# Optimization experiments

Measured on AMD Instinct MI355X. Metric: run time of the kernel, lower is better.

## Reference

```python
import jax, jax.numpy as jnp
from jax import lax
import numpy as np

B, C, H, W = 16, 192, 128, 128
NF = 192


def hard_sigmoid(x):
    # Keras 1.x hard_sigmoid: clip(0.2*x + 0.5, 0, 1)
    return jnp.clip(0.2 * x + 0.5, 0.0, 1.0)


def setup_inputs() -> dict:
    key = jax.random.key(0)
    k1, k2, k3 = jax.random.split(key, 3)
    x = jax.random.normal(k1, (B, C, H, W), dtype=jnp.float32)
    W_iof = jax.random.normal(k2, (4 * NF, C, 1, 1), dtype=jnp.float32) * 0.05
    U_iof = jax.random.normal(k3, (4 * NF, NF, 3, 1), dtype=jnp.float32) * 0.05
    b_iof = jnp.zeros((4 * NF,), dtype=jnp.float32)
    init_h = jnp.zeros((NF, W), dtype=jnp.float32)
    init_c = jnp.zeros((NF, W), dtype=jnp.float32)
    return {"x": x, "W_iof": W_iof, "U_iof": U_iof, "b_iof": b_iof,
            "init_h": init_h, "init_c": init_c}


def reference(x, W_iof, U_iof, b_iof, init_h, init_c):
    b, c, h_dim, w_dim = x.shape
    nf = init_h.shape[0]
    in3 = c // 3
    out3 = nf // 3
    # pyramid channel mask on the 1x1 input-to-state weights
    mask = jnp.ones((4 * nf, c), dtype=x.dtype)
    mask = mask.at[:out3, in3:].set(0.0)
    mask = mask.at[out3:2 * out3, 2 * in3:].set(0.0)
    Wm = W_iof[:, :, 0, 0] * mask  # (4nf, c)
    U = U_iof[:, :, :, 0]          # (4nf, nf, 3)

    # direction 'Down': scan over rows (H). Precompute input-to-state for all rows.
    X = jnp.transpose(x, (0, 2, 1, 3))  # (B, H, C, W)
    i2s = jnp.einsum('bhcw,oc->bhow', X, Wm) + b_iof[None, None, :, None]  # (B,H,4nf,W)

    h0 = jnp.broadcast_to(init_h[None], (b, nf, w_dim))
    c0 = jnp.broadcast_to(init_c[None], (b, nf, w_dim))

    def step(carry, its):
        h_tm1, c_tm1 = carry
        # 3-wide cross-correlation along W, 'half' padding (lax conv is correlation)
        s2s = lax.conv_general_dilated(h_tm1, U, (1,), [(1, 1)],
                                       dimension_numbers=('NCH', 'OIH', 'NCH'))
        gates = its + s2s  # (B, 4nf, W)
        ofi = hard_sigmoid(gates[:, :3 * nf])
        o = ofi[:, :nf]
        f = ofi[:, nf:2 * nf]
        i = ofi[:, 2 * nf:3 * nf]
        g = jnp.tanh(gates[:, 3 * nf:])
        c_new = f * c_tm1 + i * g
        h_new = o * jnp.tanh(c_new)
        return (h_new, c_new), h_new

    _, hs = lax.scan(step, (h0, c0), jnp.transpose(i2s, (1, 0, 2, 3)))  # (H,B,nf,W)
    # return_sequences=True then permute (0,2,1,3): (B, H, nf, W) -> (B, nf, H, W)
    return jnp.transpose(hs, (1, 2, 0, 3))
```

## Files before the change

### kernel.cpp

```cpp
#include <hip/hip_runtime.h>
#include <math.h>

#define BB 16
#define CC 192
#define NF 192
#define HH 128
#define WW 128
#define G4 768
#define KTOT 768
#define LDA 776
#define NJB 12
#define GRIDSZ (NJB * BB)
#define SMEM_BYTES ((64 * LDA + 128 * 24) * 2)

typedef __bf16 bf16x8 __attribute__((ext_vector_type(8)));
typedef float  f32x4  __attribute__((ext_vector_type(4)));

__device__ unsigned g_cnt[BB * 64];

__device__ __forceinline__ float hsig(float v) {
    float y = fmaf(0.2f, v, 0.5f);
    return fminf(fmaxf(y, 0.f), 1.f);
}

__device__ __forceinline__ float tanh_fast(float x) {
    float y = fminf(fmaxf(x, -8.f), 8.f) * 2.885390082f;
    float e = __builtin_amdgcn_exp2f(y);
    float r = __builtin_amdgcn_rcpf(e + 1.f);
    return fmaf(-2.f, r, 1.f);
}

__device__ __forceinline__ unsigned short f2bf(float f) {
    unsigned int u = __float_as_uint(f);
    u += 0x7fffu + ((u >> 16) & 1u);
    return (unsigned short)(u >> 16);
}

__global__ void prep_weights(const float* __restrict__ Wf,
                             const float* __restrict__ Uf,
                             unsigned short* __restrict__ Wc) {
    int idx = blockIdx.x * blockDim.x + threadIdx.x;
    if (idx < BB)
        g_cnt[idx * 64] = 0u;
    if (idx >= G4 * KTOT) return;
    int row = idx / KTOT;
    int k   = idx - row * KTOT;
    float v;
    if (k < CC) {
        int lim = row < 64 ? 64 : (row < 128 ? 128 : 192);
        v = (k < lim) ? Wf[row * CC + k] : 0.f;
    } else {
        int kp = k - CC;
        int d  = kp / CC;
        int c  = kp - d * CC;
        v = Uf[((size_t)row * CC + c) * 3 + d];
    }
    Wc[idx] = f2bf(v);
}

__global__ void prep_bx(const float* __restrict__ x, unsigned short* __restrict__ Bsrc) {
    int idx = blockIdx.x * blockDim.x + threadIdx.x;
    if (idx >= HH * BB * WW) return;
    int w = idx & (WW - 1);
    int r = idx >> 7;
    int b = r & (BB - 1);
    int t = r >> 4;
    const float* xp = x + ((size_t)b * CC * HH + t) * WW + w;
    unsigned short* dp = Bsrc + (size_t)idx * KTOT;
#pragma unroll
    for (int cc = 0; cc < CC / 8; ++cc) {
        unsigned short v[8];
#pragma unroll
        for (int i = 0; i < 8; ++i)
            v[i] = f2bf(xp[(size_t)(cc * 8 + i) * (HH * WW)]);
        *(uint4*)(dp + cc * 8) = *(uint4*)v;
    }
}

__global__ void prep_bh_oob(unsigned short* __restrict__ Bsrc) {
    int idx = blockIdx.x * blockDim.x + threadIdx.x;
    if (idx >= HH * BB * 384) return;
    int u = idx % 384;
    int r = idx / 384;
    int b = r & (BB - 1);
    int t = r >> 4;
    size_t base = ((size_t)(t * BB + b) * WW) * KTOT;
    size_t off = (u < 192) ? (size_t)0 * KTOT + 192 + u
                           : (size_t)127 * KTOT + 384 + u;
    Bsrc[base + off] = 0;
}

__global__ void prep_bh0(const float* __restrict__ init_h, unsigned short* __restrict__ Bsrc) {
    int idx = blockIdx.x * blockDim.x + threadIdx.x;
    if (idx >= BB * WW * 576) return;
    int kp = idx % 576;
    int r  = idx / 576;
    int w  = r & (WW - 1);
    int b  = r >> 7;
    int d  = kp / CC;
    int c  = kp - d * CC;
    int wt = w + d - 1;
    float v = (wt >= 0 && wt < WW) ? init_h[c * WW + wt] : 0.f;
    Bsrc[((size_t)b * WW + w) * KTOT + CC + kp] = f2bf(v);
}

__global__ __launch_bounds__(512, 1) void lstm_persist(
    const unsigned short* __restrict__ Wc,
    unsigned short* __restrict__ Bsrc,
    const float* __restrict__ bias,
    const float* __restrict__ init_c,
    float* __restrict__ out)
{
    extern __shared__ unsigned short smem[];
    unsigned short (*Alds)[LDA] = (unsigned short(*)[LDA])smem;
    unsigned short (*hT)[24]    = (unsigned short(*)[24])(smem + 64 * LDA);

    const int tid  = threadIdx.x;
    const int nw   = tid >> 6;
    const int lane = tid & 63;
    const int m    = lane & 15;
    const int q    = lane >> 4;
    const int jb   = blockIdx.x % NJB;
    const int b    = blockIdx.x / NJB;
    const int j0   = jb * 16;
    const int w    = nw * 16 + m;
    unsigned* const cntp = &g_cnt[b * 64];

    for (int u = tid; u < 64 * 96; u += 512) {
        int r  = u / 96;
        int ko = (u - r * 96) * 8;
        int grow = (r >> 4) * NF + j0 + (r & 15);
        *(uint4*)&Alds[r][ko] = *(const uint4*)(Wc + (size_t)grow * KTOT + ko);
    }
    float breg[4][4];
#pragma unroll
    for (int g = 0; g < 4; ++g)
#pragma unroll
        for (int r = 0; r < 4; ++r)
            breg[g][r] = bias[g * NF + j0 + q * 4 + r];
    float creg[4];
#pragma unroll
    for (int r = 0; r < 4; ++r)
        creg[r] = init_c[(j0 + q * 4 + r) * WW + w];
    __syncthreads();

    for (int t = 0; t < HH; ++t) {
        f32x4 acc[4];
#pragma unroll
        for (int g = 0; g < 4; ++g)
            acc[g] = (f32x4){breg[g][0], breg[g][1], breg[g][2], breg[g][3]};

        const unsigned short* Bn =
            Bsrc + ((size_t)(t * BB + b) * WW + w) * KTOT;

        bf16x8 bx[6];
#pragma unroll
        for (int kc = 0; kc < 6; ++kc)
            bx[kc] = *(const bf16x8*)(Bn + kc * 32 + q * 8);
#pragma unroll
        for (int kc = 0; kc < 6; ++kc) {
            const int k = kc * 32 + q * 8;
            bf16x8 a0 = *(const bf16x8*)&Alds[ 0 + m][k];
            bf16x8 a1 = *(const bf16x8*)&Alds[16 + m][k];
            bf16x8 a2 = *(const bf16x8*)&Alds[32 + m][k];
            bf16x8 a3 = *(const bf16x8*)&Alds[48 + m][k];
            acc[0] = __builtin_amdgcn_mfma_f32_16x16x32_bf16(a0, bx[kc], acc[0], 0, 0, 0);
            acc[1] = __builtin_amdgcn_mfma_f32_16x16x32_bf16(a1, bx[kc], acc[1], 0, 0, 0);
            acc[2] = __builtin_amdgcn_mfma_f32_16x16x32_bf16(a2, bx[kc], acc[2], 0, 0, 0);
            acc[3] = __builtin_amdgcn_mfma_f32_16x16x32_bf16(a3, bx[kc], acc[3], 0, 0, 0);
        }

        if (t > 0) {
            const unsigned need = (unsigned)(NJB * t);
            while (__hip_atomic_load(cntp, __ATOMIC_RELAXED,
                                     __HIP_MEMORY_SCOPE_AGENT) < need)
                __builtin_amdgcn_s_sleep(1);
            __builtin_amdgcn_fence(__ATOMIC_ACQUIRE, "workgroup");
        }

        bf16x8 bh[18];
#pragma unroll
        for (int kc = 0; kc < 18; ++kc)
            bh[kc] = *(const bf16x8*)(Bn + 192 + kc * 32 + q * 8);
#pragma unroll
        for (int kc = 0; kc < 18; ++kc) {
            const int k = 192 + kc * 32 + q * 8;
            bf16x8 a0 = *(const bf16x8*)&Alds[ 0 + m][k];
            bf16x8 a1 = *(const bf16x8*)&Alds[16 + m][k];
            bf16x8 a2 = *(const bf16x8*)&Alds[32 + m][k];
            bf16x8 a3 = *(const bf16x8*)&Alds[48 + m][k];
            acc[0] = __builtin_amdgcn_mfma_f32_16x16x32_bf16(a0, bh[kc], acc[0], 0, 0, 0);
            acc[1] = __builtin_amdgcn_mfma_f32_16x16x32_bf16(a1, bh[kc], acc[1], 0, 0, 0);
            acc[2] = __builtin_amdgcn_mfma_f32_16x16x32_bf16(a2, bh[kc], acc[2], 0, 0, 0);
            acc[3] = __builtin_amdgcn_mfma_f32_16x16x32_bf16(a3, bh[kc], acc[3], 0, 0, 0);
        }

#pragma unroll
        for (int r = 0; r < 4; ++r) {
            const int j = j0 + q * 4 + r;
            float og = hsig(acc[0][r]);
            float fg = hsig(acc[1][r]);
            float ig = hsig(acc[2][r]);
            float gg = tanh_fast(acc[3][r]);
            float cn = fmaf(fg, creg[r], ig * gg);
            creg[r] = cn;
            float hn = og * tanh_fast(cn);
            out[(((size_t)b * NF + j) * HH + t) * WW + w] = hn;
            hT[w][q * 4 + r] = f2bf(hn);
        }
        __syncthreads();

        if (t < HH - 1) {
            unsigned short* Bns = Bsrc + ((size_t)((t + 1) * BB + b) * WW) * KTOT;
            if (tid < 384) {
                int d  = tid >> 7;
                int w2 = tid & 127;
                int ws = w2 + d - 1;
                if (ws >= 0 && ws < WW) {
                    const unsigned long long* s8 =
                        (const unsigned long long*)&hT[ws][0];
                    unsigned long long* d8 = (unsigned long long*)
                        (Bns + (size_t)w2 * KTOT + CC + d * CC + j0);
#pragma unroll
                    for (int e = 0; e < 4; ++e)
                        __hip_atomic_store(d8 + e, s8[e], __ATOMIC_RELAXED,
                                           __HIP_MEMORY_SCOPE_AGENT);
                }
            }
            __syncthreads();
            if (tid == 0)
                __hip_atomic_fetch_add(cntp, 1u, __ATOMIC_RELAXED,
                                       __HIP_MEMORY_SCOPE_AGENT);
        }
    }
}

extern "C" void kernel_launch(void* const* d_in, const int* in_sizes, int n_in,
                              void* d_out, int out_size, void* d_ws, size_t ws_size,
                              hipStream_t stream) {
    const float* x      = (const float*)d_in[0];
    const float* W_iof  = (const float*)d_in[1];
    const float* U_iof  = (const float*)d_in[2];
    const float* b_iof  = (const float*)d_in[3];
    const float* init_h = (const float*)d_in[4];
    const float* init_c = (const float*)d_in[5];
    float* out = (float*)d_out;

    unsigned short* Wc   = (unsigned short*)d_ws;
    unsigned short* Bsrc = Wc + (size_t)G4 * KTOT;

    prep_weights<<<(G4 * KTOT + 255) / 256, 256, 0, stream>>>(W_iof, U_iof, Wc);
    prep_bx<<<(HH * BB * WW + 255) / 256, 256, 0, stream>>>(x, Bsrc);
    prep_bh_oob<<<(HH * BB * 384 + 255) / 256, 256, 0, stream>>>(Bsrc);
    prep_bh0<<<(BB * WW * 576 + 255) / 256, 256, 0, stream>>>(init_h, Bsrc);

    const unsigned short* Wcp = Wc;
    unsigned short* Bsp = Bsrc;
    const float* bp = b_iof;
    const float* icp = init_c;
    float* op = out;
    void* args[] = {&Wcp, &Bsp, &bp, &icp, &op};
    hipLaunchCooperativeKernel((const void*)lstm_persist, dim3(GRIDSZ), dim3(512),
                               args, SMEM_BYTES, stream);
}
```

Measured before the change: 1.765 ms.

## Scatter h directly from registers, prefetch next-step input, defer output store

Each thread now packs its four bf16 h values and writes them straight to the three shifted positions in the next step's B buffer. This removes the LDS staging array and one __syncthreads per step. The input-projection operand for the next timestep is prefetched into registers during the current step, and the fp32 output store is moved after the counter increment so it is off the critical path. The added s_waitcnt before the barrier keeps visibility ordering, at the cost of more scattered 8-byte global stores and more registers in use.

```diff
diff --git a/kernel.cpp b/kernel.cpp
--- a/kernel.cpp
+++ b/kernel.cpp
@@ -11,7 +11,7 @@
 #define LDA 776
 #define NJB 12
 #define GRIDSZ (NJB * BB)
-#define SMEM_BYTES ((64 * LDA + 128 * 24) * 2)
+#define SMEM_BYTES (64 * LDA * 2)
 
 typedef __bf16 bf16x8 __attribute__((ext_vector_type(8)));
 typedef float  f32x4  __attribute__((ext_vector_type(4)));
@@ -113,7 +113,6 @@
 {
     extern __shared__ unsigned short smem[];
     unsigned short (*Alds)[LDA] = (unsigned short(*)[LDA])smem;
-    unsigned short (*hT)[24]    = (unsigned short(*)[24])(smem + 64 * LDA);
 
     const int tid  = threadIdx.x;
     const int nw   = tid >> 6;
@@ -144,6 +143,14 @@
         creg[r] = init_c[(j0 + q * 4 + r) * WW + w];
     __syncthreads();
 
+    bf16x8 bxc[6], bxn[6];
+    {
+        const unsigned short* B0 = Bsrc + ((size_t)b * WW + w) * KTOT;
+#pragma unroll
+        for (int kc = 0; kc < 6; ++kc)
+            bxc[kc] = *(const bf16x8*)(B0 + kc * 32 + q * 8);
+    }
+
     for (int t = 0; t < HH; ++t) {
         f32x4 acc[4];
 #pragma unroll
@@ -153,10 +160,6 @@
         const unsigned short* Bn =
             Bsrc + ((size_t)(t * BB + b) * WW + w) * KTOT;
 
-        bf16x8 bx[6];
-#pragma unroll
-        for (int kc = 0; kc < 6; ++kc)
-            bx[kc] = *(const bf16x8*)(Bn + kc * 32 + q * 8);
 #pragma unroll
         for (int kc = 0; kc < 6; ++kc) {
             const int k = kc * 32 + q * 8;
@@ -164,10 +167,10 @@
             bf16x8 a1 = *(const bf16x8*)&Alds[16 + m][k];
             bf16x8 a2 = *(const bf16x8*)&Alds[32 + m][k];
             bf16x8 a3 = *(const bf16x8*)&Alds[48 + m][k];
-            acc[0] = __builtin_amdgcn_mfma_f32_16x16x32_bf16(a0, bx[kc], acc[0], 0, 0, 0);
-            acc[1] = __builtin_amdgcn_mfma_f32_16x16x32_bf16(a1, bx[kc], acc[1], 0, 0, 0);
-            acc[2] = __builtin_amdgcn_mfma_f32_16x16x32_bf16(a2, bx[kc], acc[2], 0, 0, 0);
-            acc[3] = __builtin_amdgcn_mfma_f32_16x16x32_bf16(a3, bx[kc], acc[3], 0, 0, 0);
+            acc[0] = __builtin_amdgcn_mfma_f32_16x16x32_bf16(a0, bxc[kc], acc[0], 0, 0, 0);
+            acc[1] = __builtin_amdgcn_mfma_f32_16x16x32_bf16(a1, bxc[kc], acc[1], 0, 0, 0);
+            acc[2] = __builtin_amdgcn_mfma_f32_16x16x32_bf16(a2, bxc[kc], acc[2], 0, 0, 0);
+            acc[3] = __builtin_amdgcn_mfma_f32_16x16x32_bf16(a3, bxc[kc], acc[3], 0, 0, 0);
         }
 
         if (t > 0) {
@@ -182,6 +185,14 @@
 #pragma unroll
         for (int kc = 0; kc < 18; ++kc)
             bh[kc] = *(const bf16x8*)(Bn + 192 + kc * 32 + q * 8);
+
+        if (t < HH - 1) {
+            const unsigned short* Bx = Bn + (size_t)BB * WW * KTOT;
+#pragma unroll
+            for (int kc = 0; kc < 6; ++kc)
+                bxn[kc] = *(const bf16x8*)(Bx + kc * 32 + q * 8);
+        }
+
 #pragma unroll
         for (int kc = 0; kc < 18; ++kc) {
             const int k = 192 + kc * 32 + q * 8;
@@ -195,43 +206,52 @@
             acc[3] = __builtin_amdgcn_mfma_f32_16x16x32_bf16(a3, bh[kc], acc[3], 0, 0, 0);
         }
 
+        float hn[4];
 #pragma unroll
         for (int r = 0; r < 4; ++r) {
-            const int j = j0 + q * 4 + r;
             float og = hsig(acc[0][r]);
             float fg = hsig(acc[1][r]);
             float ig = hsig(acc[2][r]);
             float gg = tanh_fast(acc[3][r]);
             float cn = fmaf(fg, creg[r], ig * gg);
             creg[r] = cn;
-            float hn = og * tanh_fast(cn);
-            out[(((size_t)b * NF + j) * HH + t) * WW + w] = hn;
-            hT[w][q * 4 + r] = f2bf(hn);
-        }
-        __syncthreads();
+            hn[r] = og * tanh_fast(cn);
+        }
 
         if (t < HH - 1) {
-            unsigned short* Bns = Bsrc + ((size_t)((t + 1) * BB + b) * WW) * KTOT;
-            if (tid < 384) {
-                int d  = tid >> 7;
-                int w2 = tid & 127;
-                int ws = w2 + d - 1;
-                if (ws >= 0 && ws < WW) {
-                    const unsigned long long* s8 =
-                        (const unsigned long long*)&hT[ws][0];
-                    unsigned long long* d8 = (unsigned long long*)
-                        (Bns + (size_t)w2 * KTOT + CC + d * CC + j0);
-#pragma unroll
-                    for (int e = 0; e < 4; ++e)
-                        __hip_atomic_store(d8 + e, s8[e], __ATOMIC_RELAXED,
-                                           __HIP_MEMORY_SCOPE_AGENT);
-                }
-            }
+            unsigned long long pk =
+                  (unsigned long long)f2bf(hn[0])
+                | ((unsigned long long)f2bf(hn[1]) << 16)
+                | ((unsigned long long)f2bf(hn[2]) << 32)
+                | ((unsigned long long)f2bf(hn[3]) << 48);
+            unsigned short* Bns =
+                Bsrc + ((size_t)((t + 1) * BB + b) * WW) * KTOT;
+            const int jo = CC + j0 + q * 4;
+            __hip_atomic_store((unsigned long long*)
+                (Bns + (size_t)w * KTOT + jo + CC), pk,
+                __ATOMIC_RELAXED, __HIP_MEMORY_SCOPE_AGENT);
+            if (w < WW - 1)
+                __hip_atomic_store((unsigned long long*)
+                    (Bns + (size_t)(w + 1) * KTOT + jo), pk,
+                    __ATOMIC_RELAXED, __HIP_MEMORY_SCOPE_AGENT);
+            if (w > 0)
+                __hip_atomic_store((unsigned long long*)
+                    (Bns + (size_t)(w - 1) * KTOT + jo + 2 * CC), pk,
+                    __ATOMIC_RELAXED, __HIP_MEMORY_SCOPE_AGENT);
+            asm volatile("s_waitcnt vmcnt(0)" ::: "memory");
             __syncthreads();
             if (tid == 0)
                 __hip_atomic_fetch_add(cntp, 1u, __ATOMIC_RELAXED,
                                        __HIP_MEMORY_SCOPE_AGENT);
         }
+
+#pragma unroll
+        for (int r = 0; r < 4; ++r)
+            out[(((size_t)b * NF + j0 + q * 4 + r) * HH + t) * WW + w] = hn[r];
+
+#pragma unroll
+        for (int kc = 0; kc < 6; ++kc)
+            bxc[kc] = bxn[kc];
     }
 }
 
```

Result: faster. 1.459 ms (-17.3%).
